# Performance work log

Measured on AMD Instinct MI355X. Metric: run time of the kernel, lower is better.

Reference implementation:

```python
import jax, jax.numpy as jnp
import numpy as np

F_BINS, NCH, NSRC, W, H, T, B = 257, 8, 2, 5, 32, 2000, 4
PAD = (W - 1) // 2  # use_pad=True


def setup_inputs() -> dict:
    key = jax.random.key(0)
    ks = jax.random.split(key, 7)
    s = 0.05
    return {
        "x": jax.random.normal(ks[0], (B, 2 * F_BINS, NCH, T), dtype=jnp.float32),
        # per-frequency depthwise complex conv weights: (F, Cout, Cin, w)
        "Wr1": jax.random.normal(ks[1], (F_BINS, H, NCH, W), dtype=jnp.float32) * s,
        "Wi1": jax.random.normal(ks[2], (F_BINS, H, NCH, W), dtype=jnp.float32) * s,
        "Wr2": jax.random.normal(ks[3], (F_BINS, H, H, W), dtype=jnp.float32) * s,
        "Wi2": jax.random.normal(ks[4], (F_BINS, H, H, W), dtype=jnp.float32) * s,
        "Wr3": jax.random.normal(ks[5], (F_BINS, NCH * NSRC, H, W), dtype=jnp.float32) * s,
        "Wi3": jax.random.normal(ks[6], (F_BINS, NCH * NSRC, H, W), dtype=jnp.float32) * s,
    }


def _dwconv(z, Wt):
    # z: (B, F, Cin, T) treated as NCHW with C=F, H=Cin, W=T
    # Wt: (F, Cout, Cin, w) -> grouped conv with groups=F, kernel spans full Cin
    f, cout, cin, w = Wt.shape
    k = Wt.reshape(f * cout, 1, cin, w)
    y = jax.lax.conv_general_dilated(
        z, k, window_strides=(1, 1), padding=[(0, 0), (PAD, PAD)],
        feature_group_count=f, dimension_numbers=("NCHW", "OIHW", "NCHW"))
    b = z.shape[0]
    return y.reshape(b, f, cout, -1)  # (B, F, Cout, T)


def _cconv(zr, zi, Wr, Wi):
    # complex conv: (Wr + i Wi) * (zr + i zi)
    hr = _dwconv(zr, Wr) - _dwconv(zi, Wi)
    hi = _dwconv(zr, Wi) + _dwconv(zi, Wr)
    return hr, hi


def reference(x, Wr1, Wi1, Wr2, Wi2, Wr3, Wi3):
    xr, xi = jnp.split(x, 2, axis=1)  # each (B, F, nCH, T)
    h1r, h1i = _cconv(xr, xi, Wr1, Wi1)
    h1r, h1i = jax.nn.relu(h1r), jax.nn.relu(h1i)
    h2r, h2i = _cconv(h1r, h1i, Wr2, Wi2)
    h2r, h2i = jax.nn.relu(h2r), jax.nn.relu(h2i)
    h3r, h3i = _cconv(h2r, h2i, Wr3, Wi3)  # (B, F, nCH*nSource, T)
    b, f, _, t = xr.shape
    hr = h3r.reshape(b, f, NCH, NSRC, t)
    hi = h3i.reshape(b, f, NCH, NSRC, t)
    # broadcast-multiply and reduce over channels (nCH)
    yrr = jnp.einsum("bfct,bfcst->bfst", xr, hr)
    yri = jnp.einsum("bfct,bfcst->bfst", xr, hi)
    yir = jnp.einsum("bfct,bfcst->bfst", xi, hr)
    yii = jnp.einsum("bfct,bfcst->bfst", xi, hi)
    Yr = yrr - yii
    Yi = yri + yir
    out = jnp.concatenate((Yr, Yi), axis=1)  # (B, 2F, nSource, T); squeeze is a no-op for B>1
    return jnp.squeeze(out)
```

## Files before the change

kernel.cpp:

```cpp
#include <hip/hip_runtime.h>

#define F_BINS 257
#define NCH    8
#define NSRC   2
#define KW     5
#define HCH    32
#define TLEN   2000
#define BATCH  4

#define TT      112
#define NTILES  18
#define NK      (BATCH * F_BINS)
#define NRANK   ((NK + 7) / 8)
#define GRID    (NRANK * NTILES * 8)

#define XSTRIDE 24
#define XCOLS   132
#define HWIN    128
#define HSZ     (HWIN * 64 * 2)
#define H1OFF   0
#define XOFF    HSZ
#define H2OFF   HSZ
#define H3OFF   0
#define SMEM_BYTES (2 * HSZ)
#define H3STRIDE 40

#define NFRAG   36
#define PW_HALF8_PER_F (NFRAG * 2 * 64)
#define PW_BYTES ((size_t)F_BINS * PW_HALF8_PER_F * 16)

typedef _Float16 half8  __attribute__((ext_vector_type(8)));
typedef __fp16   pk16x2 __attribute__((ext_vector_type(2)));
typedef __fp16   pk16x4 __attribute__((ext_vector_type(4)));
typedef float    f32x4  __attribute__((ext_vector_type(4)));

#define MFMA16(a, b, c) __builtin_amdgcn_mfma_f32_16x16x32_f16(a, b, c, 0, 0, 0)

__device__ __forceinline__ half8 gather_frag(
    int f, int frag, int mw, int lane,
    const float* __restrict__ Wr1, const float* __restrict__ Wi1,
    const float* __restrict__ Wr2, const float* __restrict__ Wi2,
    const float* __restrict__ Wr3, const float* __restrict__ Wi3)
{
    const int g = lane >> 4, r16 = lane & 15;
    half8 v;
    if (frag < 6) {
        int hr = frag / 3, p = frag % 3;
        int tap = 2 * p + (g >> 1);
        #pragma unroll
        for (int j = 0; j < 8; ++j) {
            float val = 0.f;
            if (tap < KW) {
                long idx = (((long)f * HCH + hr * 16 + r16) * NCH + j) * KW + tap;
                if (mw == 0) val = (g & 1) ? -Wi1[idx] : Wr1[idx];
                else         val = (g & 1) ?  Wr1[idx] : Wi1[idx];
            }
            v[j] = (_Float16)val;
        }
    } else if (frag < 26) {
        int u = frag - 6;
        int w = u >> 2, hr = (u >> 1) & 1, kk = u & 1;
        #pragma unroll
        for (int j = 0; j < 8; ++j) {
            int c = g * 8 + j;
            long idx = (((long)f * HCH + hr * 16 + r16) * HCH + c) * KW + w;
            float val;
            if (mw == 0) val = kk ? -Wi2[idx] : Wr2[idx];
            else         val = kk ?  Wr2[idx] : Wi2[idx];
            v[j] = (_Float16)val;
        }
    } else {
        int u = frag - 26;
        int w = u >> 1, kk = u & 1;
        #pragma unroll
        for (int j = 0; j < 8; ++j) {
            int c = g * 8 + j;
            long idx = (((long)f * (NCH * NSRC) + r16) * HCH + c) * KW + w;
            float val;
            if (mw == 0) val = kk ? -Wi3[idx] : Wr3[idx];
            else         val = kk ?  Wr3[idx] : Wi3[idx];
            v[j] = (_Float16)val;
        }
    }
    return v;
}

__global__ __launch_bounds__(256) void repack_kernel(
    const float* __restrict__ Wr1, const float* __restrict__ Wi1,
    const float* __restrict__ Wr2, const float* __restrict__ Wi2,
    const float* __restrict__ Wr3, const float* __restrict__ Wi3,
    _Float16* __restrict__ pw)
{
    const int bid  = blockIdx.x;
    const int f    = bid >> 2;
    const int part = bid & 3;
    const int lane = threadIdx.x & 63;
    const int q    = threadIdx.x >> 6;
    half8* pwv = (half8*)pw;
    for (int u = part * 18 + q; u < part * 18 + 18; u += 4) {
        int frag = u >> 1, mw = u & 1;
        half8 v = gather_frag(f, frag, mw, lane, Wr1, Wi1, Wr2, Wi2, Wr3, Wi3);
        pwv[((size_t)f * (NFRAG * 2) + u) * 64 + lane] = v;
    }
}

template<bool PACKED>
__global__ __launch_bounds__(256, 4) void cddcnn_mfma_kernel(
    const float* __restrict__ x,
    const float* __restrict__ Wr1, const float* __restrict__ Wi1,
    const float* __restrict__ Wr2, const float* __restrict__ Wi2,
    const float* __restrict__ Wr3, const float* __restrict__ Wi3,
    float* __restrict__ out, const _Float16* __restrict__ pw)
{
    __shared__ __align__(16) char sm[SMEM_BYTES];

    const int tid  = threadIdx.x;
    const int lane = tid & 63;
    const int wv   = tid >> 6;
    const int g    = lane >> 4;
    const int r16  = lane & 15;

    const int bid  = blockIdx.x;
    const int xcd  = bid & 7;
    const int rt   = bid >> 3;
    const int tl   = rt % NTILES;
    const int k    = (rt / NTILES) * 8 + xcd;
    if (k >= NK) return;
    const int f    = k % F_BINS;
    const int b    = k / F_BINS;
    const int t0   = tl * TT;
    const bool interior = (tl >= 1) && (tl <= 16);

    const int colb = wv * 32 + r16;

    const half8* pwb = PACKED ? ((const half8*)pw) + (size_t)f * PW_HALF8_PER_F + lane
                              : nullptr;
    #define LOADFRAG2(fr, mww) (PACKED ? pwb[((fr) * 2 + (mww)) * 64] \
                  : gather_frag(f, (fr), (mww), lane, Wr1, Wi1, Wr2, Wi2, Wr3, Wi3))

    const long xr_base = ((long)(b * 2 * F_BINS + f) * NCH) * TLEN;
    const long xi_base = ((long)(b * 2 * F_BINS + F_BINS + f) * NCH) * TLEN;

    half8 pkr = {}, pki = {};
    if (tid < XCOLS) {
        int t = t0 - 10 + tid;
        bool ok = (t >= 0) && (t < TLEN);
        #pragma unroll
        for (int c = 0; c < 8; ++c) {
            float vr = ok ? x[xr_base + (long)c * TLEN + t] : 0.f;
            float vi = ok ? x[xi_base + (long)c * TLEN + t] : 0.f;
            pkr[c] = (_Float16)vr;
            pki[c] = (_Float16)vi;
        }
        *(half8*)(sm + XOFF + tid * (XSTRIDE * 2))      = pkr;
        *(half8*)(sm + XOFF + tid * (XSTRIDE * 2) + 16) = pki;
    }

    half8 a1[2][2][3];
    #pragma unroll
    for (int mw = 0; mw < 2; ++mw)
    #pragma unroll
    for (int hr = 0; hr < 2; ++hr)
    #pragma unroll
    for (int p = 0; p < 3; ++p)
        a1[mw][hr][p] = LOADFRAG2(hr * 3 + p, mw);
    __syncthreads();

    const int Xc = (r16 & 7) << 4;
    int woff64[2][2];
    #pragma unroll
    for (int mw = 0; mw < 2; ++mw)
    #pragma unroll
    for (int hr = 0; hr < 2; ++hr)
        woff64[mw][hr] = ((mw * 64 + hr * 32 + g * 8) ^ Xc);

    half8 a2n[2][2][2];

    {
        f32x4 acc[2][2][2] = {};
        const char* xb = sm + XOFF + (colb * XSTRIDE + (g & 1) * 8) * 2;
        #pragma unroll
        for (int p = 0; p < 3; ++p) {
            int tap = 2 * p + (g >> 1);
            if (tap > 4) tap = 4;
            const char* xbp = xb + tap * (XSTRIDE * 2);
            #pragma unroll
            for (int cbi = 0; cbi < 2; ++cbi) {
                const half8 bf = *(const half8*)(xbp + cbi * (16 * XSTRIDE * 2));
                #pragma unroll
                for (int mw = 0; mw < 2; ++mw)
                #pragma unroll
                for (int hr = 0; hr < 2; ++hr)
                    acc[cbi][mw][hr] = MFMA16(a1[mw][hr][p], bf, acc[cbi][mw][hr]);
            }
        }

        #pragma unroll
        for (int mw = 0; mw < 2; ++mw)
        #pragma unroll
        for (int hr = 0; hr < 2; ++hr)
        #pragma unroll
        for (int kk = 0; kk < 2; ++kk)
            a2n[mw][hr][kk] = LOADFRAG2(6 + hr * 2 + kk, mw);

        char* wb = sm + H1OFF + colb * 128;
        #pragma unroll
        for (int cbi = 0; cbi < 2; ++cbi) {
            int t = t0 - 8 + colb + cbi * 16;
            bool ok = interior || ((t >= 0) && (t < TLEN));
            #pragma unroll
            for (int mw = 0; mw < 2; ++mw)
            #pragma unroll
            for (int hr = 0; hr < 2; ++hr) {
                float v0 = ok ? fmaxf(acc[cbi][mw][hr][0], 0.f) : 0.f;
                float v1 = ok ? fmaxf(acc[cbi][mw][hr][1], 0.f) : 0.f;
                float v2 = ok ? fmaxf(acc[cbi][mw][hr][2], 0.f) : 0.f;
                float v3 = ok ? fmaxf(acc[cbi][mw][hr][3], 0.f) : 0.f;
                pk16x2 lo = __builtin_amdgcn_cvt_pkrtz(v0, v1);
                pk16x2 hi = __builtin_amdgcn_cvt_pkrtz(v2, v3);
                pk16x4 hv; hv[0] = lo[0]; hv[1] = lo[1]; hv[2] = hi[0]; hv[3] = hi[1];
                *(pk16x4*)(wb + cbi * 2048 + woff64[mw][hr]) = hv;
            }
        }
    }
    __syncthreads();

    half8 a3n[2][2];

    {
        f32x4 acc[2][2][2] = {};
        #pragma unroll
        for (int w = 0; w < KW; ++w) {
            half8 a2c[2][2][2];
            #pragma unroll
            for (int mw = 0; mw < 2; ++mw)
            #pragma unroll
            for (int hr = 0; hr < 2; ++hr)
            #pragma unroll
            for (int kk = 0; kk < 2; ++kk)
                a2c[mw][hr][kk] = a2n[mw][hr][kk];
            if (w < 4) {
                #pragma unroll
                for (int mw = 0; mw < 2; ++mw)
                #pragma unroll
                for (int hr = 0; hr < 2; ++hr)
                #pragma unroll
                for (int kk = 0; kk < 2; ++kk)
                    a2n[mw][hr][kk] = LOADFRAG2(6 + (w + 1) * 4 + hr * 2 + kk, mw);
            }

            const int sc0 = colb + w - 2;
            const int vb  = sc0 * 128 + ((g * 16) ^ ((sc0 & 7) << 4));
            #pragma unroll
            for (int kk = 0; kk < 2; ++kk) {
                const char* rb = sm + H1OFF + (kk ? (vb ^ 64) : vb);
                #pragma unroll
                for (int cbi = 0; cbi < 2; ++cbi) {
                    const half8 bf = *(const half8*)(rb + cbi * 2048);
                    #pragma unroll
                    for (int mw = 0; mw < 2; ++mw)
                    #pragma unroll
                    for (int hr = 0; hr < 2; ++hr)
                        acc[cbi][mw][hr] = MFMA16(a2c[mw][hr][kk], bf, acc[cbi][mw][hr]);
                }
            }
        }

        #pragma unroll
        for (int mw = 0; mw < 2; ++mw)
        #pragma unroll
        for (int kk = 0; kk < 2; ++kk)
            a3n[mw][kk] = LOADFRAG2(26 + kk, mw);

        char* wb = sm + H2OFF + colb * 128;
        #pragma unroll
        for (int cbi = 0; cbi < 2; ++cbi) {
            int t = t0 - 8 + colb + cbi * 16;
            bool ok = interior || ((t >= 0) && (t < TLEN));
            #pragma unroll
            for (int mw = 0; mw < 2; ++mw)
            #pragma unroll
            for (int hr = 0; hr < 2; ++hr) {
                float v0 = ok ? fmaxf(acc[cbi][mw][hr][0], 0.f) : 0.f;
                float v1 = ok ? fmaxf(acc[cbi][mw][hr][1], 0.f) : 0.f;
                float v2 = ok ? fmaxf(acc[cbi][mw][hr][2], 0.f) : 0.f;
                float v3 = ok ? fmaxf(acc[cbi][mw][hr][3], 0.f) : 0.f;
                pk16x2 lo = __builtin_amdgcn_cvt_pkrtz(v0, v1);
                pk16x2 hi = __builtin_amdgcn_cvt_pkrtz(v2, v3);
                pk16x4 hv; hv[0] = lo[0]; hv[1] = lo[1]; hv[2] = hi[0]; hv[3] = hi[1];
                *(pk16x4*)(wb + cbi * 2048 + woff64[mw][hr]) = hv;
            }
        }
    }
    __syncthreads();

    {
        const int ncb3 = (wv == 3) ? 1 : 2;
        f32x4 acc3[2][2] = {};
        #pragma unroll
        for (int w = 0; w < KW; ++w) {
            half8 a3c[2][2];
            #pragma unroll
            for (int mw = 0; mw < 2; ++mw)
            #pragma unroll
            for (int kk = 0; kk < 2; ++kk)
                a3c[mw][kk] = a3n[mw][kk];
            if (w < 4) {
                #pragma unroll
                for (int mw = 0; mw < 2; ++mw)
                #pragma unroll
                for (int kk = 0; kk < 2; ++kk)
                    a3n[mw][kk] = LOADFRAG2(26 + (w + 1) * 2 + kk, mw);
            }

            const int sc0 = colb + 6 + w;
            const int vb  = sc0 * 128 + ((g * 16) ^ ((sc0 & 7) << 4));
            #pragma unroll
            for (int kk = 0; kk < 2; ++kk) {
                const char* rb = sm + H2OFF + (kk ? (vb ^ 64) : vb);
                #pragma unroll
                for (int cbi = 0; cbi < 2; ++cbi) {
                    if (cbi < ncb3) {
                        const half8 bf = *(const half8*)(rb + cbi * 2048);
                        #pragma unroll
                        for (int mw = 0; mw < 2; ++mw)
                            acc3[cbi][mw] = MFMA16(a3c[mw][kk], bf, acc3[cbi][mw]);
                    }
                }
            }
        }
        char* wb3 = sm + H3OFF + colb * (H3STRIDE * 2) + g * 8;
        #pragma unroll
        for (int cbi = 0; cbi < 2; ++cbi) {
            if (cbi < ncb3) {
                #pragma unroll
                for (int mw = 0; mw < 2; ++mw) {
                    pk16x2 lo = __builtin_amdgcn_cvt_pkrtz(acc3[cbi][mw][0], acc3[cbi][mw][1]);
                    pk16x2 hi = __builtin_amdgcn_cvt_pkrtz(acc3[cbi][mw][2], acc3[cbi][mw][3]);
                    pk16x4 hv; hv[0] = lo[0]; hv[1] = lo[1]; hv[2] = hi[0]; hv[3] = hi[1];
                    *(pk16x4*)(wb3 + cbi * (16 * H3STRIDE * 2) + mw * 32) = hv;
                }
            }
        }
    }
    __syncthreads();

    {
        int col = tid - 10;
        if (col >= 0 && col < TT) {
            int t = t0 + col;
            if (t < TLEN) {
                half8 h3q[4];
                #pragma unroll
                for (int q = 0; q < 4; ++q)
                    h3q[q] = *(const half8*)(sm + H3OFF + col * (H3STRIDE * 2) + q * 16);
                float Yr[2] = {0.f, 0.f}, Yi[2] = {0.f, 0.f};
                #pragma unroll
                for (int c = 0; c < NCH; ++c) {
                    float vr = (float)pkr[c];
                    float vi = (float)pki[c];
                    #pragma unroll
                    for (int s = 0; s < NSRC; ++s) {
                        int o = 2 * c + s;
                        float hr = (c < 4) ? (float)h3q[0][o] : (float)h3q[1][o - 8];
                        float hi = (c < 4) ? (float)h3q[2][o] : (float)h3q[3][o - 8];
                        Yr[s] += vr * hr - vi * hi;
                        Yi[s] += vr * hi + vi * hr;
                    }
                }
                #pragma unroll
                for (int s = 0; s < NSRC; ++s) {
                    out[((long)(b * 2 * F_BINS + f) * NSRC + s) * TLEN + t]          = Yr[s];
                    out[((long)(b * 2 * F_BINS + F_BINS + f) * NSRC + s) * TLEN + t] = Yi[s];
                }
            }
        }
    }
}

extern "C" void kernel_launch(void* const* d_in, const int* in_sizes, int n_in,
                              void* d_out, int out_size, void* d_ws, size_t ws_size,
                              hipStream_t stream) {
    const float* x   = (const float*)d_in[0];
    const float* Wr1 = (const float*)d_in[1];
    const float* Wi1 = (const float*)d_in[2];
    const float* Wr2 = (const float*)d_in[3];
    const float* Wi2 = (const float*)d_in[4];
    const float* Wr3 = (const float*)d_in[5];
    const float* Wi3 = (const float*)d_in[6];
    float* out = (float*)d_out;

    dim3 block(256);
    dim3 grid(GRID);
    if (ws_size >= PW_BYTES) {
        _Float16* pw = (_Float16*)d_ws;
        repack_kernel<<<F_BINS * 4, block, 0, stream>>>(Wr1, Wi1, Wr2, Wi2, Wr3, Wi3, pw);
        cddcnn_mfma_kernel<true><<<grid, block, 0, stream>>>(
            x, Wr1, Wi1, Wr2, Wi2, Wr3, Wi3, out, pw);
    } else {
        cddcnn_mfma_kernel<false><<<grid, block, 0, stream>>>(
            x, Wr1, Wi1, Wr2, Wi2, Wr3, Wi3, out, nullptr);
    }
}
```

Baseline: 268.0 us.

## Give each wave its own time tile and LDS region, removing block barriers

Each wave now handles its own 32-sample time tile in a private LDS slice. The block-wide __syncthreads between the three conv stages becomes a per-wave lgkmcnt wait fence, and the final stage fetches its x inputs through lane shuffles. Weight fragments are no longer prefetched one step ahead but loaded right before use, and the occupancy hint drops from 4 to 3. The cost is a larger halo per output: 52 input columns and 48 h1 columns are computed for 32 outputs, against 132 and 128 for 112 before. That means more redundant MFMA work and more weight reloads per output, plus extra zero-fill writes to LDS.

```diff
diff --git a/kernel.cpp b/kernel.cpp
--- a/kernel.cpp
+++ b/kernel.cpp
@@ -8,21 +8,18 @@
 #define TLEN   2000
 #define BATCH  4
 
-#define TT      112
-#define NTILES  18
+#define TT      32
+#define NTILES  63
+#define TGRPS   16
 #define NK      (BATCH * F_BINS)
 #define NRANK   ((NK + 7) / 8)
-#define GRID    (NRANK * NTILES * 8)
-
-#define XSTRIDE 24
-#define XCOLS   132
-#define HWIN    128
-#define HSZ     (HWIN * 64 * 2)
-#define H1OFF   0
-#define XOFF    HSZ
-#define H2OFF   HSZ
-#define H3OFF   0
-#define SMEM_BYTES (2 * HSZ)
+#define GRID    (NRANK * TGRPS * 8)
+
+#define XW      52
+#define XH2OFF  0
+#define H1OFF   6144
+#define WAVE_LDS 12544
+#define SMEM_BYTES (4 * WAVE_LDS)
 #define H3STRIDE 40
 
 #define NFRAG   36
@@ -35,6 +32,9 @@
 typedef float    f32x4  __attribute__((ext_vector_type(4)));
 
 #define MFMA16(a, b, c) __builtin_amdgcn_mfma_f32_16x16x32_f16(a, b, c, 0, 0, 0)
+
+#define WFENCE() do { asm volatile("s_waitcnt lgkmcnt(0)" ::: "memory"); \
+                      __builtin_amdgcn_sched_barrier(0); } while (0)
 
 __device__ __forceinline__ half8 gather_frag(
     int f, int frag, int mw, int lane,
@@ -105,7 +105,7 @@
 }
 
 template<bool PACKED>
-__global__ __launch_bounds__(256, 4) void cddcnn_mfma_kernel(
+__global__ __launch_bounds__(256, 3) void cddcnn_mfma_kernel(
     const float* __restrict__ x,
     const float* __restrict__ Wr1, const float* __restrict__ Wi1,
     const float* __restrict__ Wr2, const float* __restrict__ Wi2,
@@ -123,15 +123,21 @@
     const int bid  = blockIdx.x;
     const int xcd  = bid & 7;
     const int rt   = bid >> 3;
-    const int tl   = rt % NTILES;
-    const int k    = (rt / NTILES) * 8 + xcd;
+    const int tg   = rt & 15;
+    const int k    = ((rt >> 4) << 3) | xcd;
     if (k >= NK) return;
     const int f    = k % F_BINS;
     const int b    = k / F_BINS;
-    const int t0   = tl * TT;
-    const bool interior = (tl >= 1) && (tl <= 16);
-
-    const int colb = wv * 32 + r16;
+
+    const int tile = tg * 4 + wv;
+    if (tile >= NTILES) return;
+    const int t0   = tile * TT;
+    const bool interior = (tile >= 1) && (tile <= 61);
+
+    char* Wb  = sm + wv * WAVE_LDS;
+    char* Xp  = Wb + XH2OFF;
+    char* H2p = Wb + XH2OFF;
+    char* H1p = Wb + H1OFF;
 
     const half8* pwb = PACKED ? ((const half8*)pw) + (size_t)f * PW_HALF8_PER_F + lane
                               : nullptr;
@@ -141,9 +147,19 @@
     const long xr_base = ((long)(b * 2 * F_BINS + f) * NCH) * TLEN;
     const long xi_base = ((long)(b * 2 * F_BINS + F_BINS + f) * NCH) * TLEN;
 
+    {
+        half8 z = {};
+        #pragma unroll
+        for (int off = 0; off < 3648; off += 1024) {
+            int o = off + lane * 16;
+            if (o < 3648) *(half8*)(Wb + 2496 + o) = z;
+        }
+        if (lane < 16) *(half8*)(Wb + 12288 + lane * 16) = z;
+    }
+
     half8 pkr = {}, pki = {};
-    if (tid < XCOLS) {
-        int t = t0 - 10 + tid;
+    if (lane < XW) {
+        int t = t0 - 10 + lane;
         bool ok = (t >= 0) && (t < TLEN);
         #pragma unroll
         for (int c = 0; c < 8; ++c) {
@@ -152,8 +168,8 @@
             pkr[c] = (_Float16)vr;
             pki[c] = (_Float16)vi;
         }
-        *(half8*)(sm + XOFF + tid * (XSTRIDE * 2))      = pkr;
-        *(half8*)(sm + XOFF + tid * (XSTRIDE * 2) + 16) = pki;
+        *(half8*)(Xp + lane * 48)      = pkr;
+        *(half8*)(Xp + lane * 48 + 16) = pki;
     }
 
     half8 a1[2][2][3];
@@ -164,7 +180,8 @@
     #pragma unroll
     for (int p = 0; p < 3; ++p)
         a1[mw][hr][p] = LOADFRAG2(hr * 3 + p, mw);
-    __syncthreads();
+
+    WFENCE();
 
     const int Xc = (r16 & 7) << 4;
     int woff64[2][2];
@@ -174,206 +191,172 @@
     for (int hr = 0; hr < 2; ++hr)
         woff64[mw][hr] = ((mw * 64 + hr * 32 + g * 8) ^ Xc);
 
-    half8 a2n[2][2][2];
-
-    {
-        f32x4 acc[2][2][2] = {};
-        const char* xb = sm + XOFF + (colb * XSTRIDE + (g & 1) * 8) * 2;
+    {
+        f32x4 acc[3][2][2] = {};
+        const char* xb = Xp + r16 * 48 + (g & 1) * 16;
         #pragma unroll
         for (int p = 0; p < 3; ++p) {
             int tap = 2 * p + (g >> 1);
             if (tap > 4) tap = 4;
-            const char* xbp = xb + tap * (XSTRIDE * 2);
-            #pragma unroll
-            for (int cbi = 0; cbi < 2; ++cbi) {
-                const half8 bf = *(const half8*)(xbp + cbi * (16 * XSTRIDE * 2));
+            #pragma unroll
+            for (int cb = 0; cb < 3; ++cb) {
+                const half8 bf = *(const half8*)(xb + (cb * 16 + tap) * 48);
                 #pragma unroll
                 for (int mw = 0; mw < 2; ++mw)
                 #pragma unroll
                 for (int hr = 0; hr < 2; ++hr)
-                    acc[cbi][mw][hr] = MFMA16(a1[mw][hr][p], bf, acc[cbi][mw][hr]);
-            }
-        }
-
-        #pragma unroll
-        for (int mw = 0; mw < 2; ++mw)
-        #pragma unroll
-        for (int hr = 0; hr < 2; ++hr)
-        #pragma unroll
-        for (int kk = 0; kk < 2; ++kk)
-            a2n[mw][hr][kk] = LOADFRAG2(6 + hr * 2 + kk, mw);
-
-        char* wb = sm + H1OFF + colb * 128;
-        #pragma unroll
-        for (int cbi = 0; cbi < 2; ++cbi) {
-            int t = t0 - 8 + colb + cbi * 16;
+                    acc[cb][mw][hr] = MFMA16(a1[mw][hr][p], bf, acc[cb][mw][hr]);
+            }
+        }
+        #pragma unroll
+        for (int cb = 0; cb < 3; ++cb) {
+            int col = cb * 16 + r16;
+            int t = t0 - 8 + col;
             bool ok = interior || ((t >= 0) && (t < TLEN));
+            char* wb = H1p + col * 128;
             #pragma unroll
             for (int mw = 0; mw < 2; ++mw)
             #pragma unroll
             for (int hr = 0; hr < 2; ++hr) {
-                float v0 = ok ? fmaxf(acc[cbi][mw][hr][0], 0.f) : 0.f;
-                float v1 = ok ? fmaxf(acc[cbi][mw][hr][1], 0.f) : 0.f;
-                float v2 = ok ? fmaxf(acc[cbi][mw][hr][2], 0.f) : 0.f;
-                float v3 = ok ? fmaxf(acc[cbi][mw][hr][3], 0.f) : 0.f;
+                float v0 = ok ? fmaxf(acc[cb][mw][hr][0], 0.f) : 0.f;
+                float v1 = ok ? fmaxf(acc[cb][mw][hr][1], 0.f) : 0.f;
+                float v2 = ok ? fmaxf(acc[cb][mw][hr][2], 0.f) : 0.f;
+                float v3 = ok ? fmaxf(acc[cb][mw][hr][3], 0.f) : 0.f;
                 pk16x2 lo = __builtin_amdgcn_cvt_pkrtz(v0, v1);
                 pk16x2 hi = __builtin_amdgcn_cvt_pkrtz(v2, v3);
                 pk16x4 hv; hv[0] = lo[0]; hv[1] = lo[1]; hv[2] = hi[0]; hv[3] = hi[1];
-                *(pk16x4*)(wb + cbi * 2048 + woff64[mw][hr]) = hv;
-            }
-        }
-    }
-    __syncthreads();
-
-    half8 a3n[2][2];
-
-    {
-        f32x4 acc[2][2][2] = {};
+                *(pk16x4*)(wb + woff64[mw][hr]) = hv;
+            }
+        }
+    }
+
+    WFENCE();
+
+    {
+        f32x4 acc[3][2][2] = {};
         #pragma unroll
         for (int w = 0; w < KW; ++w) {
-            half8 a2c[2][2][2];
+            half8 a2[2][2][2];
             #pragma unroll
             for (int mw = 0; mw < 2; ++mw)
             #pragma unroll
             for (int hr = 0; hr < 2; ++hr)
             #pragma unroll
             for (int kk = 0; kk < 2; ++kk)
-                a2c[mw][hr][kk] = a2n[mw][hr][kk];
-            if (w < 4) {
+                a2[mw][hr][kk] = LOADFRAG2(6 + w * 4 + hr * 2 + kk, mw);
+
+            #pragma unroll
+            for (int kk = 0; kk < 2; ++kk) {
                 #pragma unroll
-                for (int mw = 0; mw < 2; ++mw)
-                #pragma unroll
-                for (int hr = 0; hr < 2; ++hr)
-                #pragma unroll
-                for (int kk = 0; kk < 2; ++kk)
-                    a2n[mw][hr][kk] = LOADFRAG2(6 + (w + 1) * 4 + hr * 2 + kk, mw);
-            }
-
-            const int sc0 = colb + w - 2;
-            const int vb  = sc0 * 128 + ((g * 16) ^ ((sc0 & 7) << 4));
-            #pragma unroll
-            for (int kk = 0; kk < 2; ++kk) {
-                const char* rb = sm + H1OFF + (kk ? (vb ^ 64) : vb);
-                #pragma unroll
-                for (int cbi = 0; cbi < 2; ++cbi) {
-                    const half8 bf = *(const half8*)(rb + cbi * 2048);
+                for (int cb = 0; cb < 3; ++cb) {
+                    const int sc0 = cb * 16 + r16 + w - 2;
+                    const int vb  = sc0 * 128 + ((g * 16) ^ ((sc0 & 7) << 4));
+                    const char* rb = H1p + (kk ? (vb ^ 64) : vb);
+                    const half8 bf = *(const half8*)rb;
                     #pragma unroll
                     for (int mw = 0; mw < 2; ++mw)
                     #pragma unroll
                     for (int hr = 0; hr < 2; ++hr)
-                        acc[cbi][mw][hr] = MFMA16(a2c[mw][hr][kk], bf, acc[cbi][mw][hr]);
+                        acc[cb][mw][hr] = MFMA16(a2[mw][hr][kk], bf, acc[cb][mw][hr]);
                 }
             }
         }
-
-        #pragma unroll
-        for (int mw = 0; mw < 2; ++mw)
-        #pragma unroll
-        for (int kk = 0; kk < 2; ++kk)
-            a3n[mw][kk] = LOADFRAG2(26 + kk, mw);
-
-        char* wb = sm + H2OFF + colb * 128;
-        #pragma unroll
-        for (int cbi = 0; cbi < 2; ++cbi) {
-            int t = t0 - 8 + colb + cbi * 16;
+        #pragma unroll
+        for (int cb = 0; cb < 3; ++cb) {
+            int col = cb * 16 + r16;
+            int t = t0 - 8 + col;
             bool ok = interior || ((t >= 0) && (t < TLEN));
+            char* wb = H2p + col * 128;
             #pragma unroll
             for (int mw = 0; mw < 2; ++mw)
             #pragma unroll
             for (int hr = 0; hr < 2; ++hr) {
-                float v0 = ok ? fmaxf(acc[cbi][mw][hr][0], 0.f) : 0.f;
-                float v1 = ok ? fmaxf(acc[cbi][mw][hr][1], 0.f) : 0.f;
-                float v2 = ok ? fmaxf(acc[cbi][mw][hr][2], 0.f) : 0.f;
-                float v3 = ok ? fmaxf(acc[cbi][mw][hr][3], 0.f) : 0.f;
+                float v0 = ok ? fmaxf(acc[cb][mw][hr][0], 0.f) : 0.f;
+                float v1 = ok ? fmaxf(acc[cb][mw][hr][1], 0.f) : 0.f;
+                float v2 = ok ? fmaxf(acc[cb][mw][hr][2], 0.f) : 0.f;
+                float v3 = ok ? fmaxf(acc[cb][mw][hr][3], 0.f) : 0.f;
                 pk16x2 lo = __builtin_amdgcn_cvt_pkrtz(v0, v1);
                 pk16x2 hi = __builtin_amdgcn_cvt_pkrtz(v2, v3);
                 pk16x4 hv; hv[0] = lo[0]; hv[1] = lo[1]; hv[2] = hi[0]; hv[3] = hi[1];
-                *(pk16x4*)(wb + cbi * 2048 + woff64[mw][hr]) = hv;
-            }
-        }
-    }
-    __syncthreads();
-
-    {
-        const int ncb3 = (wv == 3) ? 1 : 2;
+                *(pk16x4*)(wb + woff64[mw][hr]) = hv;
+            }
+        }
+    }
+
+    WFENCE();
+
+    {
         f32x4 acc3[2][2] = {};
         #pragma unroll
         for (int w = 0; w < KW; ++w) {
-            half8 a3c[2][2];
+            half8 a3[2][2];
             #pragma unroll
             for (int mw = 0; mw < 2; ++mw)
             #pragma unroll
             for (int kk = 0; kk < 2; ++kk)
-                a3c[mw][kk] = a3n[mw][kk];
-            if (w < 4) {
+                a3[mw][kk] = LOADFRAG2(26 + w * 2 + kk, mw);
+
+            #pragma unroll
+            for (int kk = 0; kk < 2; ++kk) {
                 #pragma unroll
-                for (int mw = 0; mw < 2; ++mw)
-                #pragma unroll
-                for (int kk = 0; kk < 2; ++kk)
-                    a3n[mw][kk] = LOADFRAG2(26 + (w + 1) * 2 + kk, mw);
-            }
-
-            const int sc0 = colb + 6 + w;
-            const int vb  = sc0 * 128 + ((g * 16) ^ ((sc0 & 7) << 4));
-            #pragma unroll
-            for (int kk = 0; kk < 2; ++kk) {
-                const char* rb = sm + H2OFF + (kk ? (vb ^ 64) : vb);
-                #pragma unroll
-                for (int cbi = 0; cbi < 2; ++cbi) {
-                    if (cbi < ncb3) {
-                        const half8 bf = *(const half8*)(rb + cbi * 2048);
-                        #pragma unroll
-                        for (int mw = 0; mw < 2; ++mw)
-                            acc3[cbi][mw] = MFMA16(a3c[mw][kk], bf, acc3[cbi][mw]);
-                    }
+                for (int cb = 0; cb < 2; ++cb) {
+                    const int sc0 = cb * 16 + r16 + 6 + w;
+                    const int vb  = sc0 * 128 + ((g * 16) ^ ((sc0 & 7) << 4));
+                    const char* rb = H2p + (kk ? (vb ^ 64) : vb);
+                    const half8 bf = *(const half8*)rb;
+                    #pragma unroll
+                    for (int mw = 0; mw < 2; ++mw)
+                        acc3[cb][mw] = MFMA16(a3[mw][kk], bf, acc3[cb][mw]);
                 }
             }
         }
-        char* wb3 = sm + H3OFF + colb * (H3STRIDE * 2) + g * 8;
-        #pragma unroll
-        for (int cbi = 0; cbi < 2; ++cbi) {
-            if (cbi < ncb3) {
-                #pragma unroll
-                for (int mw = 0; mw < 2; ++mw) {
-                    pk16x2 lo = __builtin_amdgcn_cvt_pkrtz(acc3[cbi][mw][0], acc3[cbi][mw][1]);
-                    pk16x2 hi = __builtin_amdgcn_cvt_pkrtz(acc3[cbi][mw][2], acc3[cbi][mw][3]);
-                    pk16x4 hv; hv[0] = lo[0]; hv[1] = lo[1]; hv[2] = hi[0]; hv[3] = hi[1];
-                    *(pk16x4*)(wb3 + cbi * (16 * H3STRIDE * 2) + mw * 32) = hv;
-                }
-            }
-        }
-    }
-    __syncthreads();
-
-    {
-        int col = tid - 10;
-        if (col >= 0 && col < TT) {
-            int t = t0 + col;
-            if (t < TLEN) {
-                half8 h3q[4];
-                #pragma unroll
-                for (int q = 0; q < 4; ++q)
-                    h3q[q] = *(const half8*)(sm + H3OFF + col * (H3STRIDE * 2) + q * 16);
-                float Yr[2] = {0.f, 0.f}, Yi[2] = {0.f, 0.f};
-                #pragma unroll
-                for (int c = 0; c < NCH; ++c) {
-                    float vr = (float)pkr[c];
-                    float vi = (float)pki[c];
-                    #pragma unroll
-                    for (int s = 0; s < NSRC; ++s) {
-                        int o = 2 * c + s;
-                        float hr = (c < 4) ? (float)h3q[0][o] : (float)h3q[1][o - 8];
-                        float hi = (c < 4) ? (float)h3q[2][o] : (float)h3q[3][o - 8];
-                        Yr[s] += vr * hr - vi * hi;
-                        Yi[s] += vr * hi + vi * hr;
-                    }
-                }
-                #pragma unroll
-                for (int s = 0; s < NSRC; ++s) {
-                    out[((long)(b * 2 * F_BINS + f) * NSRC + s) * TLEN + t]          = Yr[s];
-                    out[((long)(b * 2 * F_BINS + F_BINS + f) * NSRC + s) * TLEN + t] = Yi[s];
-                }
-            }
+        #pragma unroll
+        for (int cb = 0; cb < 2; ++cb) {
+            char* wb3 = H1p + (cb * 16 + r16) * (H3STRIDE * 2) + g * 8;
+            #pragma unroll
+            for (int mw = 0; mw < 2; ++mw) {
+                pk16x2 lo = __builtin_amdgcn_cvt_pkrtz(acc3[cb][mw][0], acc3[cb][mw][1]);
+                pk16x2 hi = __builtin_amdgcn_cvt_pkrtz(acc3[cb][mw][2], acc3[cb][mw][3]);
+                pk16x4 hv; hv[0] = lo[0]; hv[1] = lo[1]; hv[2] = hi[0]; hv[3] = hi[1];
+                *(pk16x4*)(wb3 + mw * 32) = hv;
+            }
+        }
+    }
+
+    WFENCE();
+
+    {
+        int s   = lane >> 5;
+        int col = lane & 31;
+        int t   = t0 + col;
+        int src = col + 10;
+        int4 ir = *reinterpret_cast<int4*>(&pkr);
+        int4 ii = *reinterpret_cast<int4*>(&pki);
+        int4 jr, ji;
+        jr.x = __shfl(ir.x, src); jr.y = __shfl(ir.y, src);
+        jr.z = __shfl(ir.z, src); jr.w = __shfl(ir.w, src);
+        ji.x = __shfl(ii.x, src); ji.y = __shfl(ii.y, src);
+        ji.z = __shfl(ii.z, src); ji.w = __shfl(ii.w, src);
+        half8 xr8 = *reinterpret_cast<half8*>(&jr);
+        half8 xi8 = *reinterpret_cast<half8*>(&ji);
+        if (t < TLEN) {
+            half8 h3q[4];
+            #pragma unroll
+            for (int q = 0; q < 4; ++q)
+                h3q[q] = *(const half8*)(H1p + col * (H3STRIDE * 2) + q * 16);
+            float Yr = 0.f, Yi = 0.f;
+            #pragma unroll
+            for (int c = 0; c < NCH; ++c) {
+                float vr = (float)xr8[c];
+                float vi = (float)xi8[c];
+                int o = 2 * c + s;
+                float hr = (c < 4) ? (float)h3q[0][o] : (float)h3q[1][o - 8];
+                float hi = (c < 4) ? (float)h3q[2][o] : (float)h3q[3][o - 8];
+                Yr += vr * hr - vi * hi;
+                Yi += vr * hi + vi * hr;
+            }
+            out[((long)(b * 2 * F_BINS + f) * NSRC + s) * TLEN + t]          = Yr;
+            out[((long)(b * 2 * F_BINS + F_BINS + f) * NSRC + s) * TLEN + t] = Yi;
         }
     }
 }
```

Result: slower. 344.4 us (+28.5%).
